# Performance work log

Measured on AMD Instinct MI355X. Metric: run time of the kernel, lower is better.

## Reference

```python
import jax, jax.numpy as jnp
import numpy as np

B, C, H, W = 4, 64, 64, 64


def setup_inputs() -> dict:
    key = jax.random.key(0)
    k1, k2, k3, k4, k5 = jax.random.split(key, 5)
    return {
        "x": jax.random.normal(k1, (B, C, H, W), dtype=jnp.float32),
        "w_qkv": jax.random.normal(k2, (3 * C, C), dtype=jnp.float32) * (1.0 / np.sqrt(C)),
        "b_qkv": jax.random.normal(k3, (3 * C,), dtype=jnp.float32) * 0.02,
        "w_proj": jax.random.normal(k4, (C, C), dtype=jnp.float32) * (1.0 / np.sqrt(C)),
        "b_proj": jax.random.normal(k5, (C,), dtype=jnp.float32) * 0.02,
    }


def reference(x, w_qkv, b_qkv, w_proj, b_proj):
    b, c, h, w = x.shape
    xf = x.reshape(b, c, h * w)                                  # [B, C, N]
    # 1x1 Conv1d == per-position linear over channels
    qkv = jnp.einsum('oc,bcn->bon', w_qkv, xf) + b_qkv[None, :, None]  # [B, 3C, N]
    q, k, v = jnp.split(qkv, 3, axis=1)                          # each [B, C, N]
    scores = jnp.einsum('bcn,bcm->bnm', q, k) / (c ** 0.5)       # [B, N, N]
    attn = jax.nn.softmax(scores, axis=-1)
    out = jnp.einsum('bcm,bnm->bcn', v, attn)                    # [B, C, N]
    out = jnp.einsum('oc,bcn->bon', w_proj, out) + b_proj[None, :, None]
    return out.reshape(b, c, h, w) + x
```

## Files before the change

kernel.cpp:

```cpp
#include <hip/hip_runtime.h>

typedef __bf16 bf16x8 __attribute__((ext_vector_type(8)));
typedef __bf16 bf16x4 __attribute__((ext_vector_type(4)));
typedef __bf16 bf16x2 __attribute__((ext_vector_type(2)));
typedef float f32x4 __attribute__((ext_vector_type(4)));

#define NB 4
#define NC 64
#define NN 4096
#define SPLIT 8

#define QSCALE (0.125f * 1.44269504088896340736f)

__global__ __launch_bounds__(256) void qkv_kernel(
    const float* __restrict__ x, const float* __restrict__ wqkv,
    const float* __restrict__ bqkv,
    __bf16* __restrict__ Qg, __bf16* __restrict__ Kg, __bf16* __restrict__ Vg)
{
  const int tid = threadIdx.x;
  const int b = blockIdx.y;
  const int z = blockIdx.z;
  const int tsel = z >> 3;
  const int obase = (z & 7) * 8;
  const int n = blockIdx.x * 512 + tid * 2;
  const float wscale = (tsel == 0) ? QSCALE : 1.0f;

  __shared__ float wsh[8 * 64];
  __shared__ float bsh[8];
  wsh[tid]       = wqkv[(tsel * 64 + obase) * 64 + tid] * wscale;
  wsh[tid + 256] = wqkv[(tsel * 64 + obase) * 64 + tid + 256] * wscale;
  if (tid < 8) bsh[tid] = bqkv[tsel * 64 + obase + tid] * wscale;
  __syncthreads();

  float xa[64], xb[64];
#pragma unroll
  for (int c = 0; c < 64; c++) {
    const float2 t = *(const float2*)&x[((size_t)(b * 64 + c)) * NN + n];
    xa[c] = t.x; xb[c] = t.y;
  }

  float aa[8], ab[8];
#pragma unroll
  for (int j = 0; j < 8; j++) { aa[j] = bsh[j]; ab[j] = bsh[j]; }
#pragma unroll
  for (int c4 = 0; c4 < 64; c4 += 4) {
#pragma unroll
    for (int j = 0; j < 8; j++) {
      const float4 wv = *(const float4*)&wsh[j * 64 + c4];
      aa[j] = fmaf(wv.x, xa[c4 + 0], aa[j]);
      aa[j] = fmaf(wv.y, xa[c4 + 1], aa[j]);
      aa[j] = fmaf(wv.z, xa[c4 + 2], aa[j]);
      aa[j] = fmaf(wv.w, xa[c4 + 3], aa[j]);
      ab[j] = fmaf(wv.x, xb[c4 + 0], ab[j]);
      ab[j] = fmaf(wv.y, xb[c4 + 1], ab[j]);
      ab[j] = fmaf(wv.z, xb[c4 + 2], ab[j]);
      ab[j] = fmaf(wv.w, xb[c4 + 3], ab[j]);
    }
  }

  if (tsel == 2) {
#pragma unroll
    for (int j = 0; j < 8; j++) {
      bf16x2 pv;
      pv[0] = (__bf16)aa[j]; pv[1] = (__bf16)ab[j];
      *(bf16x2*)(Vg + ((size_t)(b * 64 + obase + j)) * NN + n) = pv;
    }
  } else {
    __bf16* base = (tsel == 0 ? Qg : Kg);
    bf16x8 p0, p1;
#pragma unroll
    for (int j = 0; j < 8; j++) { p0[j] = (__bf16)aa[j]; p1[j] = (__bf16)ab[j]; }
    *(bf16x8*)(base + ((size_t)(b * NN + n)) * 64 + obase) = p0;
    *(bf16x8*)(base + ((size_t)(b * NN + n + 1)) * 64 + obase) = p1;
  }
}

__global__ __launch_bounds__(256) void flash_kernel(
    const __bf16* __restrict__ Q, const __bf16* __restrict__ K,
    const __bf16* __restrict__ V, __bf16* __restrict__ Opart,
    float* __restrict__ lpart)
{
  const int b = blockIdx.y;
  const int s = blockIdx.z;
  const int tid = threadIdx.x;
  const int wave = tid >> 6;
  const int lane = tid & 63;
  const int quad = lane >> 4;
  const int l16 = lane & 15;

  __shared__ __bf16 Kt[64 * 72];
  __shared__ __bf16 Vt[64 * 72];
  __shared__ __bf16 Pt[4][32 * 72];

  const int q0 = blockIdx.x * 128 + wave * 32;

  bf16x8 qf[2][2];
#pragma unroll
  for (int qt = 0; qt < 2; qt++) {
    const __bf16* qrow = Q + ((size_t)(b * NN + q0 + qt * 16 + l16)) * 64;
    qf[qt][0] = *(const bf16x8*)(qrow + quad * 8);
    qf[qt][1] = *(const bf16x8*)(qrow + 32 + quad * 8);
  }

  f32x4 acc[2][4];
#pragma unroll
  for (int qt = 0; qt < 2; qt++)
#pragma unroll
    for (int ct = 0; ct < 4; ct++) acc[qt][ct] = (f32x4){0.f, 0.f, 0.f, 0.f};
  float l[2] = {0.f, 0.f};

  const int kbeg = s * (NN / SPLIT);
  const int kend = kbeg + (NN / SPLIT);
  for (int kt0 = kbeg; kt0 < kend; kt0 += 64) {
    __syncthreads();
#pragma unroll
    for (int it = 0; it < 2; it++) {
      const int chunk = tid + it * 256;
      const int row = chunk >> 3, col8 = (chunk & 7) * 8;
      *(bf16x8*)(&Kt[row * 72 + col8]) =
          *(const bf16x8*)(K + ((size_t)(b * NN + kt0 + row)) * 64 + col8);
      *(bf16x8*)(&Vt[row * 72 + col8]) =
          *(const bf16x8*)(V + ((size_t)(b * 64 + row)) * NN + kt0 + col8);
    }
    __syncthreads();

#pragma unroll
    for (int t = 0; t < 4; t++) {
      const bf16x8 kf0 = *(const bf16x8*)(&Kt[(t * 16 + l16) * 72 + quad * 8]);
      const bf16x8 kf1 = *(const bf16x8*)(&Kt[(t * 16 + l16) * 72 + 32 + quad * 8]);
#pragma unroll
      for (int qt = 0; qt < 2; qt++) {
        f32x4 z = (f32x4){0.f, 0.f, 0.f, 0.f};
        z = __builtin_amdgcn_mfma_f32_16x16x32_bf16(kf0, qf[qt][0], z, 0, 0, 0);
        z = __builtin_amdgcn_mfma_f32_16x16x32_bf16(kf1, qf[qt][1], z, 0, 0, 0);
        const float p0 = exp2f(z[0]), p1 = exp2f(z[1]);
        const float p2 = exp2f(z[2]), p3 = exp2f(z[3]);
        l[qt] += (p0 + p1) + (p2 + p3);
        bf16x4 pk;
        pk[0] = (__bf16)p0; pk[1] = (__bf16)p1;
        pk[2] = (__bf16)p2; pk[3] = (__bf16)p3;
        *(bf16x4*)(&Pt[wave][(qt * 16 + l16) * 72 + t * 16 + quad * 4]) = pk;
      }
    }

#pragma unroll
    for (int kb = 0; kb < 2; kb++) {
      const bf16x8 pf0 = *(const bf16x8*)(&Pt[wave][l16 * 72 + kb * 32 + quad * 8]);
      const bf16x8 pf1 = *(const bf16x8*)(&Pt[wave][(16 + l16) * 72 + kb * 32 + quad * 8]);
#pragma unroll
      for (int ct = 0; ct < 4; ct++) {
        const bf16x8 vf = *(const bf16x8*)(&Vt[(ct * 16 + l16) * 72 + kb * 32 + quad * 8]);
        acc[0][ct] = __builtin_amdgcn_mfma_f32_16x16x32_bf16(vf, pf0, acc[0][ct], 0, 0, 0);
        acc[1][ct] = __builtin_amdgcn_mfma_f32_16x16x32_bf16(vf, pf1, acc[1][ct], 0, 0, 0);
      }
    }
  }

#pragma unroll
  for (int qt = 0; qt < 2; qt++) {
    float lr = l[qt];
    lr += __shfl_xor(lr, 16);
    lr += __shfl_xor(lr, 32);
    if (quad == 0)
      lpart[((size_t)(s * NB + b)) * NN + q0 + qt * 16 + l16] = lr;
#pragma unroll
    for (int ct = 0; ct < 4; ct++)
#pragma unroll
      for (int r = 0; r < 4; r++)
        Opart[(((size_t)(s * NB + b)) * 64 + ct * 16 + quad * 4 + r) * NN +
              q0 + qt * 16 + l16] = (__bf16)acc[qt][ct][r];
  }
}

__global__ __launch_bounds__(256) void combine_proj_kernel(
    const __bf16* __restrict__ Opart, const float* __restrict__ lpart,
    const float* __restrict__ wproj, const float* __restrict__ bproj,
    const float* __restrict__ x, float* __restrict__ out)
{
  const int b = blockIdx.y;
  const int n0 = blockIdx.x * 32;
  const int tid = threadIdx.x;

  __shared__ float Ot[64 * 36];
  __shared__ float wT[64 * 66];
  __shared__ float lsh[32];
  __shared__ float bsh[64];

  if (tid < 32) {
    float lt = 0.f;
#pragma unroll
    for (int s = 0; s < SPLIT; s++)
      lt += lpart[((size_t)(s * NB + b)) * NN + n0 + tid];
    lsh[tid] = 1.0f / lt;
  }
  if (tid < 64) bsh[tid] = bproj[tid];
#pragma unroll
  for (int k = 0; k < 16; k++) {
    const int i = tid + k * 256;
    wT[(i & 63) * 66 + (i >> 6)] = wproj[i];
  }
  __syncthreads();

  {
    const int c = tid >> 2;
    const int n8 = (tid & 3) * 8;
    float o[8];
#pragma unroll
    for (int j = 0; j < 8; j++) o[j] = 0.f;
#pragma unroll
    for (int s = 0; s < SPLIT; s++) {
      const bf16x8 v = *(const bf16x8*)(
          Opart + (((size_t)(s * NB + b)) * 64 + c) * NN + n0 + n8);
#pragma unroll
      for (int j = 0; j < 8; j++) o[j] += (float)v[j];
    }
#pragma unroll
    for (int j = 0; j < 8; j++) Ot[c * 36 + n8 + j] = o[j] * lsh[n8 + j];
  }
  __syncthreads();

  const int co = (tid >> 3) * 2;
  const int ng = (tid & 7) * 4;
  float a0[4], a1[4];
#pragma unroll
  for (int j = 0; j < 4; j++) { a0[j] = bsh[co]; a1[j] = bsh[co + 1]; }
  for (int cin = 0; cin < 64; cin++) {
    const float4 ov = *(const float4*)&Ot[cin * 36 + ng];
    const float2 wv = *(const float2*)&wT[cin * 66 + co];
    a0[0] = fmaf(wv.x, ov.x, a0[0]); a0[1] = fmaf(wv.x, ov.y, a0[1]);
    a0[2] = fmaf(wv.x, ov.z, a0[2]); a0[3] = fmaf(wv.x, ov.w, a0[3]);
    a1[0] = fmaf(wv.y, ov.x, a1[0]); a1[1] = fmaf(wv.y, ov.y, a1[1]);
    a1[2] = fmaf(wv.y, ov.z, a1[2]); a1[3] = fmaf(wv.y, ov.w, a1[3]);
  }

#pragma unroll
  for (int i = 0; i < 2; i++) {
    float* ai = (i == 0) ? a0 : a1;
    const size_t base = ((size_t)(b * 64 + co + i)) * NN + n0 + ng;
    const float4 xr = *(const float4*)&x[base];
    float4 r;
    r.x = ai[0] + xr.x; r.y = ai[1] + xr.y;
    r.z = ai[2] + xr.z; r.w = ai[3] + xr.w;
    *(float4*)&out[base] = r;
  }
}

extern "C" void kernel_launch(void* const* d_in, const int* in_sizes, int n_in,
                              void* d_out, int out_size, void* d_ws, size_t ws_size,
                              hipStream_t stream) {
  const float* x     = (const float*)d_in[0];
  const float* wqkv  = (const float*)d_in[1];
  const float* bqkv  = (const float*)d_in[2];
  const float* wproj = (const float*)d_in[3];
  const float* bproj = (const float*)d_in[4];
  float* out = (float*)d_out;

  char* ws = (char*)d_ws;
  __bf16* Q     = (__bf16*)(ws);
  __bf16* K     = (__bf16*)(ws + (2u << 20));
  __bf16* V     = (__bf16*)(ws + (4u << 20));
  __bf16* Opart = (__bf16*)(ws + (6u << 20));
  float*  lpart = (float*)(ws + (23u << 20));

  qkv_kernel<<<dim3(8, NB, 24), 256, 0, stream>>>(x, wqkv, bqkv, Q, K, V);
  flash_kernel<<<dim3(32, NB, SPLIT), 256, 0, stream>>>(Q, K, V, Opart, lpart);
  combine_proj_kernel<<<dim3(128, NB), 256, 0, stream>>>(Opart, lpart, wproj,
                                                         bproj, x, out);
}
```

Baseline: 117.3 us.

## Load K/V fragments directly from global memory, drop shared staging and block barriers

Removes the shared-memory staging of K and V tiles and both __syncthreads per iteration. Each wave now reads its MFMA fragments for K and V straight from global memory, relying on L1/L2 to serve the four waves that read the same tile. The per-wave P scratch buffer is double-buffered so consecutive iterations do not overwrite P while it may still be read. exp2f is replaced with the hardware exp2 builtin when available. In exchange, global and cache traffic rise fourfold because tiles are no longer shared across waves, and the loads become less coalesced.

New measurement: 146.0 us. 24.4% more time.

```diff
diff --git a/kernel.cpp b/kernel.cpp
--- a/kernel.cpp
+++ b/kernel.cpp
@@ -11,6 +11,12 @@
 #define SPLIT 8
 
 #define QSCALE (0.125f * 1.44269504088896340736f)
+
+#if __has_builtin(__builtin_amdgcn_exp2f)
+#define EXP2(x) __builtin_amdgcn_exp2f(x)
+#else
+#define EXP2(x) exp2f(x)
+#endif
 
 __global__ __launch_bounds__(256) void qkv_kernel(
     const float* __restrict__ x, const float* __restrict__ wqkv,
@@ -88,9 +94,7 @@
   const int quad = lane >> 4;
   const int l16 = lane & 15;
 
-  __shared__ __bf16 Kt[64 * 72];
-  __shared__ __bf16 Vt[64 * 72];
-  __shared__ __bf16 Pt[4][32 * 72];
+  __shared__ __bf16 Pt[4][2][32 * 72];
 
   const int q0 = blockIdx.x * 128 + wave * 32;
 
@@ -110,46 +114,40 @@
   float l[2] = {0.f, 0.f};
 
   const int kbeg = s * (NN / SPLIT);
-  const int kend = kbeg + (NN / SPLIT);
-  for (int kt0 = kbeg; kt0 < kend; kt0 += 64) {
-    __syncthreads();
-#pragma unroll
-    for (int it = 0; it < 2; it++) {
-      const int chunk = tid + it * 256;
-      const int row = chunk >> 3, col8 = (chunk & 7) * 8;
-      *(bf16x8*)(&Kt[row * 72 + col8]) =
-          *(const bf16x8*)(K + ((size_t)(b * NN + kt0 + row)) * 64 + col8);
-      *(bf16x8*)(&Vt[row * 72 + col8]) =
-          *(const bf16x8*)(V + ((size_t)(b * 64 + row)) * NN + kt0 + col8);
-    }
-    __syncthreads();
+  const int ntiles = (NN / SPLIT) / 64;
+#pragma unroll 1
+  for (int it = 0; it < ntiles; it++) {
+    const int kt0 = kbeg + it * 64;
+    __bf16* P = Pt[wave][it & 1];
 
 #pragma unroll
     for (int t = 0; t < 4; t++) {
-      const bf16x8 kf0 = *(const bf16x8*)(&Kt[(t * 16 + l16) * 72 + quad * 8]);
-      const bf16x8 kf1 = *(const bf16x8*)(&Kt[(t * 16 + l16) * 72 + 32 + quad * 8]);
+      const __bf16* krow = K + ((size_t)(b * NN + kt0 + t * 16 + l16)) * 64 + quad * 8;
+      const bf16x8 kf0 = *(const bf16x8*)(krow);
+      const bf16x8 kf1 = *(const bf16x8*)(krow + 32);
 #pragma unroll
       for (int qt = 0; qt < 2; qt++) {
         f32x4 z = (f32x4){0.f, 0.f, 0.f, 0.f};
         z = __builtin_amdgcn_mfma_f32_16x16x32_bf16(kf0, qf[qt][0], z, 0, 0, 0);
         z = __builtin_amdgcn_mfma_f32_16x16x32_bf16(kf1, qf[qt][1], z, 0, 0, 0);
-        const float p0 = exp2f(z[0]), p1 = exp2f(z[1]);
-        const float p2 = exp2f(z[2]), p3 = exp2f(z[3]);
+        const float p0 = EXP2(z[0]), p1 = EXP2(z[1]);
+        const float p2 = EXP2(z[2]), p3 = EXP2(z[3]);
         l[qt] += (p0 + p1) + (p2 + p3);
         bf16x4 pk;
         pk[0] = (__bf16)p0; pk[1] = (__bf16)p1;
         pk[2] = (__bf16)p2; pk[3] = (__bf16)p3;
-        *(bf16x4*)(&Pt[wave][(qt * 16 + l16) * 72 + t * 16 + quad * 4]) = pk;
+        *(bf16x4*)(&P[(qt * 16 + l16) * 72 + t * 16 + quad * 4]) = pk;
       }
     }
 
 #pragma unroll
     for (int kb = 0; kb < 2; kb++) {
-      const bf16x8 pf0 = *(const bf16x8*)(&Pt[wave][l16 * 72 + kb * 32 + quad * 8]);
-      const bf16x8 pf1 = *(const bf16x8*)(&Pt[wave][(16 + l16) * 72 + kb * 32 + quad * 8]);
+      const bf16x8 pf0 = *(const bf16x8*)(&P[l16 * 72 + kb * 32 + quad * 8]);
+      const bf16x8 pf1 = *(const bf16x8*)(&P[(16 + l16) * 72 + kb * 32 + quad * 8]);
 #pragma unroll
       for (int ct = 0; ct < 4; ct++) {
-        const bf16x8 vf = *(const bf16x8*)(&Vt[(ct * 16 + l16) * 72 + kb * 32 + quad * 8]);
+        const bf16x8 vf = *(const bf16x8*)(
+            V + ((size_t)(b * 64 + ct * 16 + l16)) * NN + kt0 + kb * 32 + quad * 8);
         acc[0][ct] = __builtin_amdgcn_mfma_f32_16x16x32_bf16(vf, pf0, acc[0][ct], 0, 0, 0);
         acc[1][ct] = __builtin_amdgcn_mfma_f32_16x16x32_bf16(vf, pf1, acc[1][ct], 0, 0, 0);
       }
```

## Keep softmax probabilities in registers, feeding PV MFMA directly via 16x16x16 layout

Applied to the files above, without the earlier changes.

Drops the per-wave LDS staging buffer for the probability tile. The exp'd scores stay in registers and feed 16x16x16 bf16 MFMAs, whose operand layout matches the QK output fragment, so the LDS store/load round trip and its shared memory go away. It also switches exp2f to the hardware exp2 builtin and keeps the outer loop from unrolling. The cost is twice as many smaller MFMA instructions with half-width V loads, and the exp2 builtin skips the denormal range handling of exp2f.

After: 113.7 us. 1.03x faster.

```diff
diff --git a/kernel.cpp b/kernel.cpp
--- a/kernel.cpp
+++ b/kernel.cpp
@@ -4,6 +4,7 @@
 typedef __bf16 bf16x4 __attribute__((ext_vector_type(4)));
 typedef __bf16 bf16x2 __attribute__((ext_vector_type(2)));
 typedef float f32x4 __attribute__((ext_vector_type(4)));
+typedef short s16x4 __attribute__((ext_vector_type(4)));
 
 #define NB 4
 #define NC 64
@@ -11,6 +12,12 @@
 #define SPLIT 8
 
 #define QSCALE (0.125f * 1.44269504088896340736f)
+
+#if __has_builtin(__builtin_amdgcn_exp2f)
+#define EXP2(x) __builtin_amdgcn_exp2f(x)
+#else
+#define EXP2(x) exp2f(x)
+#endif
 
 __global__ __launch_bounds__(256) void qkv_kernel(
     const float* __restrict__ x, const float* __restrict__ wqkv,
@@ -90,7 +97,6 @@
 
   __shared__ __bf16 Kt[64 * 72];
   __shared__ __bf16 Vt[64 * 72];
-  __shared__ __bf16 Pt[4][32 * 72];
 
   const int q0 = blockIdx.x * 128 + wave * 32;
 
@@ -111,6 +117,7 @@
 
   const int kbeg = s * (NN / SPLIT);
   const int kend = kbeg + (NN / SPLIT);
+#pragma unroll 1
   for (int kt0 = kbeg; kt0 < kend; kt0 += 64) {
     __syncthreads();
 #pragma unroll
@@ -124,6 +131,7 @@
     }
     __syncthreads();
 
+    s16x4 pk[4][2];
 #pragma unroll
     for (int t = 0; t < 4; t++) {
       const bf16x8 kf0 = *(const bf16x8*)(&Kt[(t * 16 + l16) * 72 + quad * 8]);
@@ -133,25 +141,27 @@
         f32x4 z = (f32x4){0.f, 0.f, 0.f, 0.f};
         z = __builtin_amdgcn_mfma_f32_16x16x32_bf16(kf0, qf[qt][0], z, 0, 0, 0);
         z = __builtin_amdgcn_mfma_f32_16x16x32_bf16(kf1, qf[qt][1], z, 0, 0, 0);
-        const float p0 = exp2f(z[0]), p1 = exp2f(z[1]);
-        const float p2 = exp2f(z[2]), p3 = exp2f(z[3]);
+        const float p0 = EXP2(z[0]), p1 = EXP2(z[1]);
+        const float p2 = EXP2(z[2]), p3 = EXP2(z[3]);
         l[qt] += (p0 + p1) + (p2 + p3);
-        bf16x4 pk;
-        pk[0] = (__bf16)p0; pk[1] = (__bf16)p1;
-        pk[2] = (__bf16)p2; pk[3] = (__bf16)p3;
-        *(bf16x4*)(&Pt[wave][(qt * 16 + l16) * 72 + t * 16 + quad * 4]) = pk;
+        bf16x4 pv;
+        pv[0] = (__bf16)p0; pv[1] = (__bf16)p1;
+        pv[2] = (__bf16)p2; pv[3] = (__bf16)p3;
+        pk[t][qt] = __builtin_bit_cast(s16x4, pv);
       }
     }
 
 #pragma unroll
-    for (int kb = 0; kb < 2; kb++) {
-      const bf16x8 pf0 = *(const bf16x8*)(&Pt[wave][l16 * 72 + kb * 32 + quad * 8]);
-      const bf16x8 pf1 = *(const bf16x8*)(&Pt[wave][(16 + l16) * 72 + kb * 32 + quad * 8]);
+    for (int kg = 0; kg < 4; kg++) {
 #pragma unroll
       for (int ct = 0; ct < 4; ct++) {
-        const bf16x8 vf = *(const bf16x8*)(&Vt[(ct * 16 + l16) * 72 + kb * 32 + quad * 8]);
-        acc[0][ct] = __builtin_amdgcn_mfma_f32_16x16x32_bf16(vf, pf0, acc[0][ct], 0, 0, 0);
-        acc[1][ct] = __builtin_amdgcn_mfma_f32_16x16x32_bf16(vf, pf1, acc[1][ct], 0, 0, 0);
+        const bf16x4 va =
+            *(const bf16x4*)(&Vt[(ct * 16 + l16) * 72 + kg * 16 + quad * 4]);
+        const s16x4 a = __builtin_bit_cast(s16x4, va);
+        acc[0][ct] = __builtin_amdgcn_mfma_f32_16x16x16bf16_1k(
+            a, pk[kg][0], acc[0][ct], 0, 0, 0);
+        acc[1][ct] = __builtin_amdgcn_mfma_f32_16x16x16bf16_1k(
+            a, pk[kg][1], acc[1][ct], 0, 0, 0);
       }
     }
   }
```
